# Optimization experiments

Measured on AMD Instinct MI355X. Metric: run time of the kernel, lower is better.

## Reference

```python
import jax, jax.numpy as jnp
import numpy as np

B, C, H, W, K = 16, 512, 64, 64, 64  # K = external-attention latent dim (self.k = 64)


def setup_inputs() -> dict:
    key = jax.random.key(0)
    ks = jax.random.split(key, 5)
    x = jax.random.normal(ks[0], (B, C, H, W), dtype=jnp.float32)
    # conv1: Conv2d(c, c, 1) with bias; init normal(0, sqrt(2/(1*1*out_channels)))
    conv1_w = jax.random.normal(ks[1], (C, C), dtype=jnp.float32) * np.float32(np.sqrt(2.0 / C))
    conv1_b = jnp.zeros((C,), dtype=jnp.float32)
    # linear_0: Conv1d(c, k, 1, bias=False); init normal(0, sqrt(2/out_channels))
    lin0_w = jax.random.normal(ks[2], (K, C), dtype=jnp.float32) * np.float32(np.sqrt(2.0 / K))
    # linear_1: Conv1d(k, c, 1, bias=False)
    lin1_w = jax.random.normal(ks[3], (C, K), dtype=jnp.float32) * np.float32(np.sqrt(2.0 / C))
    # conv2: Conv2d(c, c, 1, bias=False)
    conv2_w = jax.random.normal(ks[4], (C, C), dtype=jnp.float32) * np.float32(np.sqrt(2.0 / C))
    return {"x": x, "conv1_w": conv1_w, "conv1_b": conv1_b,
            "lin0_w": lin0_w, "lin1_w": lin1_w, "conv2_w": conv2_w}


def reference(x, conv1_w, conv1_b, lin0_w, lin1_w, conv2_w):
    b, c, h, w = x.shape
    n = h * w
    idn = x
    # conv1: 1x1 conv == per-pixel GEMM
    y = jnp.einsum('oc,bchw->bohw', conv1_w, x) + conv1_b[None, :, None, None]
    y = y.reshape(b, c, n)
    # external attention: linear_0 -> softmax over tokens -> L1 renorm over latent dim
    attn = jnp.einsum('kc,bcn->bkn', lin0_w, y)          # (b, K, n)
    attn = jax.nn.softmax(attn, axis=-1)
    attn = attn / (1e-9 + attn.sum(axis=1, keepdims=True))
    y = jnp.einsum('ck,bkn->bcn', lin1_w, attn)          # (b, c, n)
    # rank: view(-1, c) row-major (as torch .view does), per-row topk threshold,
    # scale below-threshold by 0.75 and the rest by 1.25; output is detached
    # (torch.tensor(pred, requires_grad=False)) -> stop_gradient
    top_k = c // 2
    flat = y.reshape(-1, c)                               # (b*n, c) row-major chunks
    thr = jax.lax.top_k(flat, top_k)[0][:, -1:]           # k-th largest per row
    scaled = jnp.where(flat < thr, 0.75 * flat, 1.25 * flat)
    yr = jax.lax.stop_gradient(scaled).reshape(b, c, h, w)
    # conv2: 1x1 conv no bias + ReLU, residual add, final ReLU
    out = jax.nn.relu(jnp.einsum('oc,bchw->bohw', conv2_w, yr))
    return jax.nn.relu(out + idn)
```

## Files before the change

### kernel.cpp

```cpp
#include <hip/hip_runtime.h>
#include <stdint.h>

typedef unsigned short u16;
typedef unsigned int u32;
using short8 = __attribute__((ext_vector_type(8))) short;
using f32x4  = __attribute__((ext_vector_type(4))) float;

#define BDIM 16
#define CDIM 512
#define KLAT 64
#define NTOK 4096

__device__ __forceinline__ u16 f2bf(float x) {
  union { float f; u32 u; } a; a.f = x;
  u32 r = a.u + 0x7FFFu + ((a.u >> 16) & 1u);
  return (u16)(r >> 16);
}
__device__ __forceinline__ u32 pack2(float a, float b) {
  return (u32)f2bf(a) | ((u32)f2bf(b) << 16);
}
__device__ __forceinline__ u32 f2key(float x) {
  u32 u = __float_as_uint(x);
  return (u & 0x80000000u) ? ~u : (u | 0x80000000u);
}
__device__ __forceinline__ float keyscale(u32 k_, u32 thr) {
  u32 u = (k_ & 0x80000000u) ? (k_ & 0x7FFFFFFFu) : ~k_;
  float v = __uint_as_float(u);
  return (k_ < thr) ? 0.75f * v : 1.25f * v;
}
__device__ __forceinline__ void gload_lds16(const void* g, void* l) {
  __builtin_amdgcn_global_load_lds(
      (const __attribute__((address_space(1))) unsigned int*)g,
      (__attribute__((address_space(3))) unsigned int*)l, 16, 0, 0);
}

__global__ __launch_bounds__(256) void k_setup(
    const float* __restrict__ conv1_w, const float* __restrict__ conv1_b,
    const float* __restrict__ lin0_w,  const float* __restrict__ lin1_w,
    const float* __restrict__ conv2_w,
    u16* __restrict__ w0bf, float* __restrict__ b0,
    u16* __restrict__ lin1bf, u16* __restrict__ cwbf)
{
  const int bid = blockIdx.x;
  const int t = threadIdx.x;
  if (bid < 128) {
    const int kb = bid & 15, cb = bid >> 4;
    const int lane = t & 63;
    int k = kb * 4 + (t >> 6);
    k = __builtin_amdgcn_readfirstlane(k);
    const int c = cb * 64 + lane;
    float acc = 0.f;
    const float* l0 = lin0_w + (size_t)k * CDIM;
    const float* cw = conv1_w + c;
#pragma unroll 4
    for (int o = 0; o < CDIM; ++o)
      acc = fmaf(l0[o], cw[(size_t)o * CDIM], acc);
    w0bf[k * CDIM + c] = f2bf(acc);
  } else if (bid == 128) {
    if (t < KLAT) {
      float acc = 0.f;
      for (int c = 0; c < CDIM; ++c) acc = fmaf(lin0_w[t * CDIM + c], conv1_b[c], acc);
      b0[t] = acc;
    }
  } else if (bid < 193) {
    const int b2 = bid - 129;
    const float4* src = (const float4*)conv2_w;
#pragma unroll
    for (int i = 0; i < 4; ++i) {
      int idx = (b2 * 256 + t) + i * 16384;
      float4 v = src[idx];
      uint2 o;
      o.x = pack2(v.x, v.y);
      o.y = pack2(v.z, v.w);
      *(uint2*)(cwbf + (size_t)idx * 4) = o;
    }
  } else {
    const int b2 = bid - 193;
#pragma unroll
    for (int i = 0; i < 4; ++i) {
      int g = b2 * 1024 + i * 256 + t;
      float4 v0 = *(const float4*)(lin1_w + (size_t)g * 8);
      float4 v1 = *(const float4*)(lin1_w + (size_t)g * 8 + 4);
      uint4 o;
      o.x = pack2(v0.x, v0.y); o.y = pack2(v0.z, v0.w);
      o.z = pack2(v1.x, v1.y); o.w = pack2(v1.z, v1.w);
      *(uint4*)(lin1bf + (size_t)g * 8) = o;
    }
  }
}

__global__ __launch_bounds__(256) void k_logits(
    const u16* __restrict__ w0bf, const float* __restrict__ x,
    const float* __restrict__ b0, float* __restrict__ logits)
{
  __shared__ u16 As[64 * 72];
  __shared__ float xt[64 * 128];
  const int nb = blockIdx.x, b = blockIdx.y;
  const int t = threadIdx.x;
  const int wv = t >> 6, lane = t & 63;
  const int quad = lane >> 4, l15 = lane & 15;
  f32x4 acc[4][2];
#pragma unroll
  for (int mi = 0; mi < 4; ++mi)
#pragma unroll
    for (int ni = 0; ni < 2; ++ni) acc[mi][ni] = (f32x4){0.f, 0.f, 0.f, 0.f};

  for (int kc = 0; kc < 8; ++kc) {
#pragma unroll
    for (int i = 0; i < 2; ++i) {
      int ch = t + i * 256;
      int row = ch >> 3, col = (ch & 7) * 8;
      uint4 a = *(const uint4*)(w0bf + (size_t)row * CDIM + kc * 64 + col);
      *(uint4*)&As[row * 72 + col] = a;
    }
#pragma unroll
    for (int i = 0; i < 8; ++i) {
      int f4 = t + i * 256;
      int row = f4 >> 5, col4 = f4 & 31;
      float4 v = *(const float4*)(x + ((size_t)(b * CDIM + kc * 64 + row)) * NTOK
                                  + nb * 128 + col4 * 4);
      int phys4 = (col4 + row + (row >> 3)) & 31;
      *(float4*)&xt[row * 128 + phys4 * 4] = v;
    }
    __syncthreads();
#pragma unroll
    for (int kk = 0; kk < 2; ++kk) {
      short8 af[4], bf_[2];
#pragma unroll
      for (int mi = 0; mi < 4; ++mi)
        af[mi] = *(short8*)&As[(mi * 16 + l15) * 72 + kk * 32 + quad * 8];
#pragma unroll
      for (int ni = 0; ni < 2; ++ni) {
        const int n = wv * 32 + ni * 16 + l15;
        const int n4 = n >> 2, ns = n & 3;
        union { u32 u[4]; short8 s; } cvt;
#pragma unroll
        for (int jj = 0; jj < 4; ++jj) {
          int ca = kk * 32 + quad * 8 + jj * 2;
          int cb2 = ca + 1;
          float v0 = xt[ca * 128 + (((n4 + ca + (ca >> 3)) & 31) * 4) + ns];
          float v1 = xt[cb2 * 128 + (((n4 + cb2 + (cb2 >> 3)) & 31) * 4) + ns];
          cvt.u[jj] = pack2(v0, v1);
        }
        bf_[ni] = cvt.s;
      }
#pragma unroll
      for (int mi = 0; mi < 4; ++mi)
#pragma unroll
        for (int ni = 0; ni < 2; ++ni)
          acc[mi][ni] = __builtin_amdgcn_mfma_f32_16x16x32_bf16(
              af[mi], bf_[ni], acc[mi][ni], 0, 0, 0);
    }
    __syncthreads();
  }
#pragma unroll
  for (int mi = 0; mi < 4; ++mi) {
#pragma unroll
    for (int ni = 0; ni < 2; ++ni) {
#pragma unroll
      for (int r = 0; r < 4; ++r) {
        int row = mi * 16 + quad * 4 + r;
        int col = nb * 128 + wv * 32 + ni * 16 + l15;
        logits[((size_t)(b * KLAT + row)) * NTOK + col] = acc[mi][ni][r] + b0[row];
      }
    }
  }
}

__global__ __launch_bounds__(256) void k_softmax(float* __restrict__ attn)
{
  __shared__ float red[4], red2[4];
  const int t = threadIdx.x;
  float* p = attn + (size_t)blockIdx.x * NTOK;
  float4 v[4];
#pragma unroll
  for (int i = 0; i < 4; ++i) v[i] = ((float4*)p)[t + i * 256];
  float m = v[0].x;
#pragma unroll
  for (int i = 0; i < 4; ++i)
    m = fmaxf(m, fmaxf(fmaxf(v[i].x, v[i].y), fmaxf(v[i].z, v[i].w)));
#pragma unroll
  for (int o = 1; o < 64; o <<= 1) m = fmaxf(m, __shfl_xor(m, o));
  const int wv = t >> 6, lane = t & 63;
  if (lane == 0) red[wv] = m;
  __syncthreads();
  m = fmaxf(fmaxf(red[0], red[1]), fmaxf(red[2], red[3]));
  float s = 0.f;
#pragma unroll
  for (int i = 0; i < 4; ++i) {
    v[i].x = __expf(v[i].x - m); s += v[i].x;
    v[i].y = __expf(v[i].y - m); s += v[i].y;
    v[i].z = __expf(v[i].z - m); s += v[i].z;
    v[i].w = __expf(v[i].w - m); s += v[i].w;
  }
#pragma unroll
  for (int o = 1; o < 64; o <<= 1) s += __shfl_xor(s, o);
  if (lane == 0) red2[wv] = s;
  __syncthreads();
  s = red2[0] + red2[1] + red2[2] + red2[3];
  const float inv = 1.f / s;
#pragma unroll
  for (int i = 0; i < 4; ++i) {
    v[i].x *= inv; v[i].y *= inv; v[i].z *= inv; v[i].w *= inv;
    ((float4*)p)[t + i * 256] = v[i];
  }
}

__global__ __launch_bounds__(256) void k_attnT(
    const float* __restrict__ attn, u16* __restrict__ attnT)
{
  __shared__ float tile[64 * 256];
  __shared__ float inv_[256];
  const int n0 = blockIdx.x * 256, b = blockIdx.y;
  const int t = threadIdx.x;
#pragma unroll
  for (int i = 0; i < 16; ++i) {
    int f4 = t + i * 256;
    int row = f4 >> 6, col4 = f4 & 63;
    float4 v = *(const float4*)(attn + ((size_t)(b * KLAT + row)) * NTOK + n0 + col4 * 4);
    int phys4 = (col4 + row + (row >> 3)) & 63;
    *(float4*)&tile[row * 256 + phys4 * 4] = v;
  }
  __syncthreads();
  {
    int n4 = t >> 2, sub = t & 3;
    float s = 0.f;
#pragma unroll
    for (int k = 0; k < 64; ++k) {
      int phys4 = (n4 + k + (k >> 3)) & 63;
      s += tile[k * 256 + phys4 * 4 + sub];
    }
    inv_[t] = 1.f / (1e-9f + s);
  }
  __syncthreads();
#pragma unroll
  for (int i = 0; i < 8; ++i) {
    int nr = (t >> 3) + i * 32;
    int cs = (t & 7) * 8;
    float sc = inv_[nr];
    float w[8];
#pragma unroll
    for (int j = 0; j < 8; ++j) {
      int row = cs + j;
      int phys4 = ((nr >> 2) + row + (row >> 3)) & 63;
      w[j] = tile[row * 256 + phys4 * 4 + (nr & 3)] * sc;
    }
    uint4 o;
    o.x = pack2(w[0], w[1]); o.y = pack2(w[2], w[3]);
    o.z = pack2(w[4], w[5]); o.w = pack2(w[6], w[7]);
    *(uint4*)(attnT + ((size_t)(b * NTOK + n0 + nr)) * KLAT + cs) = o;
  }
}

__global__ __launch_bounds__(512) void k_lin1rank(
    const u16* __restrict__ lin1bf, const u16* __restrict__ attnT,
    u16* __restrict__ yrt)
{
  __shared__ float tile[32 * 512];
  const int n0 = blockIdx.x * 512, c0 = blockIdx.y * 32, b = blockIdx.z;
  const int t = threadIdx.x;
  const int wv = t >> 6, lane = t & 63;
  const int quad = lane >> 4, l15 = lane & 15;

  short8 af[2][2], bfr[4][2];
#pragma unroll
  for (int mi = 0; mi < 2; ++mi)
#pragma unroll
    for (int kk = 0; kk < 2; ++kk)
      af[mi][kk] = *(const short8*)(lin1bf +
          (size_t)(c0 + mi * 16 + l15) * KLAT + kk * 32 + quad * 8);
#pragma unroll
  for (int ni = 0; ni < 4; ++ni)
#pragma unroll
    for (int kk = 0; kk < 2; ++kk)
      bfr[ni][kk] = *(const short8*)(attnT +
          ((size_t)(b * NTOK + n0 + wv * 64 + ni * 16 + l15)) * KLAT + kk * 32 + quad * 8);
  f32x4 acc[2][4];
#pragma unroll
  for (int mi = 0; mi < 2; ++mi)
#pragma unroll
    for (int ni = 0; ni < 4; ++ni) acc[mi][ni] = (f32x4){0.f, 0.f, 0.f, 0.f};
#pragma unroll
  for (int kk = 0; kk < 2; ++kk)
#pragma unroll
    for (int mi = 0; mi < 2; ++mi)
#pragma unroll
      for (int ni = 0; ni < 4; ++ni)
        acc[mi][ni] = __builtin_amdgcn_mfma_f32_16x16x32_bf16(
            af[mi][kk], bfr[ni][kk], acc[mi][ni], 0, 0, 0);
#pragma unroll
  for (int mi = 0; mi < 2; ++mi) {
#pragma unroll
    for (int ni = 0; ni < 4; ++ni) {
#pragma unroll
      for (int r = 0; r < 4; ++r) {
        int row = mi * 16 + quad * 4 + r;
        int col = wv * 64 + ni * 16 + l15;
        int phys4 = ((col >> 2) + row + (row >> 3)) & 127;
        tile[row * 512 + phys4 * 4 + (col & 3)] = acc[mi][ni][r];
      }
    }
  }
  __syncthreads();

#pragma unroll
  for (int r = 0; r < 4; ++r) {
    const int row = wv * 4 + r;
    const int rot = row + (row >> 3);
    const int c4a = (lane + rot) & 127;
    const int c4b = (64 + lane + rot) & 127;
    float* pa = &tile[row * 512 + c4a * 4];
    float* pb = &tile[row * 512 + c4b * 4];
    float4 va = *(const float4*)pa;
    float4 vb = *(const float4*)pb;
    u32 key[8];
    key[0] = f2key(va.x); key[1] = f2key(va.y);
    key[2] = f2key(va.z); key[3] = f2key(va.w);
    key[4] = f2key(vb.x); key[5] = f2key(vb.y);
    key[6] = f2key(vb.z); key[7] = f2key(vb.w);
    u32 kmin = key[0], kmax = key[0];
#pragma unroll
    for (int j = 1; j < 8; ++j) {
      kmin = key[j] < kmin ? key[j] : kmin;
      kmax = key[j] > kmax ? key[j] : kmax;
    }
#pragma unroll
    for (int o = 1; o < 64; o <<= 1) {
      u32 a_ = __shfl_xor(kmin, o), b_ = __shfl_xor(kmax, o);
      kmin = a_ < kmin ? a_ : kmin;
      kmax = b_ > kmax ? b_ : kmax;
    }
    u32 lo = kmin, hi = kmax;
    u32 thr;
    if (lo >= hi) thr = lo;
    else for (;;) {
      u32 d = hi - lo;
      u32 mid = lo + (d >> 1) + (d & 1u);
      int cnt = 0;
#pragma unroll
      for (int j = 0; j < 8; ++j)
        cnt += (int)__popcll(__ballot(key[j] >= mid));
      if (cnt == 256) { thr = mid; break; }
      if (cnt > 256) lo = mid; else hi = mid - 1u;
      if (lo >= hi) { thr = lo; break; }
    }
    float4 oa, ob;
    oa.x = keyscale(key[0], thr); oa.y = keyscale(key[1], thr);
    oa.z = keyscale(key[2], thr); oa.w = keyscale(key[3], thr);
    ob.x = keyscale(key[4], thr); ob.y = keyscale(key[5], thr);
    ob.z = keyscale(key[6], thr); ob.w = keyscale(key[7], thr);
    *(float4*)pa = oa;
    *(float4*)pb = ob;
  }
  __syncthreads();

#pragma unroll
  for (int i = 0; i < 4; ++i) {
    int nr = (t >> 2) + i * 128;
    int cs = (t & 3) * 8;
    float w[8];
#pragma unroll
    for (int j = 0; j < 8; ++j) {
      int row = cs + j;
      int phys4 = ((nr >> 2) + row + (row >> 3)) & 127;
      w[j] = tile[row * 512 + phys4 * 4 + (nr & 3)];
    }
    uint4 o;
    o.x = pack2(w[0], w[1]); o.y = pack2(w[2], w[3]);
    o.z = pack2(w[4], w[5]); o.w = pack2(w[6], w[7]);
    *(uint4*)(yrt + ((size_t)(b * NTOK + n0 + nr)) * CDIM + c0 + cs) = o;
  }
}

__global__ __launch_bounds__(256) void k_conv2(
    const u16* __restrict__ cwbf, const u16* __restrict__ yrt,
    const float* __restrict__ x, float* __restrict__ out)
{
  __shared__ __align__(16) u16 smem[2 * 128 * 64];
  u16* As = smem;
  u16* Bs = smem + 128 * 64;
  float* sbuf = (float*)smem;
  const int nb = blockIdx.x, mb = blockIdx.y, b = blockIdx.z;
  const int t = threadIdx.x;
  const int wv = t >> 6, lane = t & 63;
  const int wm = wv >> 1, wn = wv & 1;
  const int quad = lane >> 4, l15 = lane & 15;
  const int lrow = lane >> 3, lg = lane & 7;
  f32x4 acc[4][4];
#pragma unroll
  for (int mi = 0; mi < 4; ++mi)
#pragma unroll
    for (int ni = 0; ni < 4; ++ni) acc[mi][ni] = (f32x4){0.f, 0.f, 0.f, 0.f};

  for (int kc = 0; kc < 8; ++kc) {
#pragma unroll
    for (int i = 0; i < 4; ++i) {
      const int r0 = i * 32 + wv * 8;
      const int row = r0 + lrow;
      const int gsrc = lg ^ (row & 7);
      const u16* ga = cwbf + ((size_t)(mb * 128 + row)) * CDIM + kc * 64 + gsrc * 8;
      gload_lds16(ga, &As[r0 * 64]);
      const u16* gb = yrt + ((size_t)(b * NTOK + nb * 128 + row)) * CDIM + kc * 64 + gsrc * 8;
      gload_lds16(gb, &Bs[r0 * 64]);
    }
    __syncthreads();
#pragma unroll
    for (int kk = 0; kk < 2; ++kk) {
      short8 af[4], bf_[4];
#pragma unroll
      for (int mi = 0; mi < 4; ++mi) {
        int row = wm * 64 + mi * 16 + l15;
        int q = kk * 4 + quad;
        af[mi] = *(short8*)&As[row * 64 + ((q ^ (row & 7)) * 8)];
      }
#pragma unroll
      for (int ni = 0; ni < 4; ++ni) {
        int row = wn * 64 + ni * 16 + l15;
        int q = kk * 4 + quad;
        bf_[ni] = *(short8*)&Bs[row * 64 + ((q ^ (row & 7)) * 8)];
      }
#pragma unroll
      for (int mi = 0; mi < 4; ++mi)
#pragma unroll
        for (int ni = 0; ni < 4; ++ni)
          acc[mi][ni] = __builtin_amdgcn_mfma_f32_16x16x32_bf16(
              af[mi], bf_[ni], acc[mi][ni], 0, 0, 0);
    }
    __syncthreads();
  }
#pragma unroll
  for (int mi = 0; mi < 4; ++mi) {
#pragma unroll
    for (int ni = 0; ni < 4; ++ni)
#pragma unroll
      for (int r = 0; r < 4; ++r)
        sbuf[(wm * 16 + quad * 4 + r) * 132 + wn * 64 + ni * 16 + l15] = acc[mi][ni][r];
    __syncthreads();
#pragma unroll
    for (int i = 0; i < 4; ++i) {
      int f4 = t + i * 256;
      int sr = f4 >> 5, sc4 = f4 & 31;
      int grow = mb * 128 + (sr >> 4) * 64 + mi * 16 + (sr & 15);
      size_t off = ((size_t)(b * CDIM + grow)) * NTOK + nb * 128 + sc4 * 4;
      float4 a4 = *(const float4*)&sbuf[sr * 132 + sc4 * 4];
      float4 xa = *(const float4*)(x + off);
      float4 o4;
      o4.x = fmaxf(fmaxf(a4.x, 0.f) + xa.x, 0.f);
      o4.y = fmaxf(fmaxf(a4.y, 0.f) + xa.y, 0.f);
      o4.z = fmaxf(fmaxf(a4.z, 0.f) + xa.z, 0.f);
      o4.w = fmaxf(fmaxf(a4.w, 0.f) + xa.w, 0.f);
      *(float4*)(out + off) = o4;
    }
    __syncthreads();
  }
}

extern "C" void kernel_launch(void* const* d_in, const int* in_sizes, int n_in,
                              void* d_out, int out_size, void* d_ws, size_t ws_size,
                              hipStream_t stream)
{
  const float* x       = (const float*)d_in[0];
  const float* conv1_w = (const float*)d_in[1];
  const float* conv1_b = (const float*)d_in[2];
  const float* lin0_w  = (const float*)d_in[3];
  const float* lin1_w  = (const float*)d_in[4];
  const float* conv2_w = (const float*)d_in[5];
  float* out = (float*)d_out;

  char* ws = (char*)d_ws;
  float* attn  = (float*)ws;
  u16*   yrt   = (u16*)(ws + 16777216);
  u16*   attnT = (u16*)d_out;
  char*  wsm   = ws + 16777216 + 67108864;
  u16*   w0bf  = (u16*)wsm;
  float* b0    = (float*)(wsm + 131072);
  u16*   lin1bf= (u16*)(wsm + 131328);
  u16*   cwbf  = (u16*)(wsm + 262400);

  k_setup   <<<197, 256, 0, stream>>>(conv1_w, conv1_b, lin0_w, lin1_w, conv2_w,
                                      w0bf, b0, lin1bf, cwbf);
  k_logits  <<<dim3(32, 16), 256, 0, stream>>>(w0bf, x, b0, attn);
  k_softmax <<<1024, 256, 0, stream>>>(attn);
  k_attnT   <<<dim3(16, 16), 256, 0, stream>>>(attn, attnT);
  k_lin1rank<<<dim3(8, 16, 16), 512, 0, stream>>>(lin1bf, attnT, yrt);
  k_conv2   <<<dim3(32, 4, 16), 256, 0, stream>>>(cwbf, yrt, x, out);
}
```

Baseline: 474.0 us.

## Load conv2 MFMA operands directly from global memory, bypassing LDS staging

```diff
diff --git a/kernel.cpp b/kernel.cpp
--- a/kernel.cpp
+++ b/kernel.cpp
@@ -27,11 +27,6 @@
   u32 u = (k_ & 0x80000000u) ? (k_ & 0x7FFFFFFFu) : ~k_;
   float v = __uint_as_float(u);
   return (k_ < thr) ? 0.75f * v : 1.25f * v;
-}
-__device__ __forceinline__ void gload_lds16(const void* g, void* l) {
-  __builtin_amdgcn_global_load_lds(
-      (const __attribute__((address_space(1))) unsigned int*)g,
-      (__attribute__((address_space(3))) unsigned int*)l, 16, 0, 0);
 }
 
 __global__ __launch_bounds__(256) void k_setup(
@@ -376,58 +371,50 @@
     const u16* __restrict__ cwbf, const u16* __restrict__ yrt,
     const float* __restrict__ x, float* __restrict__ out)
 {
-  __shared__ __align__(16) u16 smem[2 * 128 * 64];
-  u16* As = smem;
-  u16* Bs = smem + 128 * 64;
-  float* sbuf = (float*)smem;
+  __shared__ __align__(16) float sbuf[32 * 132];
   const int nb = blockIdx.x, mb = blockIdx.y, b = blockIdx.z;
   const int t = threadIdx.x;
   const int wv = t >> 6, lane = t & 63;
   const int wm = wv >> 1, wn = wv & 1;
   const int quad = lane >> 4, l15 = lane & 15;
-  const int lrow = lane >> 3, lg = lane & 7;
   f32x4 acc[4][4];
 #pragma unroll
   for (int mi = 0; mi < 4; ++mi)
 #pragma unroll
     for (int ni = 0; ni < 4; ++ni) acc[mi][ni] = (f32x4){0.f, 0.f, 0.f, 0.f};
 
+  const u16* arow[4];
+  const u16* brow[4];
+#pragma unroll
+  for (int mi = 0; mi < 4; ++mi)
+    arow[mi] = cwbf + ((size_t)(mb * 128 + wm * 64 + mi * 16 + l15)) * CDIM + quad * 8;
+#pragma unroll
+  for (int ni = 0; ni < 4; ++ni)
+    brow[ni] = yrt + ((size_t)(b * NTOK + nb * 128 + wn * 64 + ni * 16 + l15)) * CDIM + quad * 8;
+
+#pragma unroll 2
   for (int kc = 0; kc < 8; ++kc) {
-#pragma unroll
-    for (int i = 0; i < 4; ++i) {
-      const int r0 = i * 32 + wv * 8;
-      const int row = r0 + lrow;
-      const int gsrc = lg ^ (row & 7);
-      const u16* ga = cwbf + ((size_t)(mb * 128 + row)) * CDIM + kc * 64 + gsrc * 8;
-      gload_lds16(ga, &As[r0 * 64]);
-      const u16* gb = yrt + ((size_t)(b * NTOK + nb * 128 + row)) * CDIM + kc * 64 + gsrc * 8;
-      gload_lds16(gb, &Bs[r0 * 64]);
-    }
-    __syncthreads();
-#pragma unroll
-    for (int kk = 0; kk < 2; ++kk) {
-      short8 af[4], bf_[4];
-#pragma unroll
-      for (int mi = 0; mi < 4; ++mi) {
-        int row = wm * 64 + mi * 16 + l15;
-        int q = kk * 4 + quad;
-        af[mi] = *(short8*)&As[row * 64 + ((q ^ (row & 7)) * 8)];
-      }
-#pragma unroll
-      for (int ni = 0; ni < 4; ++ni) {
-        int row = wn * 64 + ni * 16 + l15;
-        int q = kk * 4 + quad;
-        bf_[ni] = *(short8*)&Bs[row * 64 + ((q ^ (row & 7)) * 8)];
-      }
+    short8 af[4][2], bf_[4][2];
+#pragma unroll
+    for (int mi = 0; mi < 4; ++mi) {
+      af[mi][0] = *(const short8*)(arow[mi] + kc * 64);
+      af[mi][1] = *(const short8*)(arow[mi] + kc * 64 + 32);
+    }
+#pragma unroll
+    for (int ni = 0; ni < 4; ++ni) {
+      bf_[ni][0] = *(const short8*)(brow[ni] + kc * 64);
+      bf_[ni][1] = *(const short8*)(brow[ni] + kc * 64 + 32);
+    }
+#pragma unroll
+    for (int kk = 0; kk < 2; ++kk)
 #pragma unroll
       for (int mi = 0; mi < 4; ++mi)
 #pragma unroll
         for (int ni = 0; ni < 4; ++ni)
           acc[mi][ni] = __builtin_amdgcn_mfma_f32_16x16x32_bf16(
-              af[mi], bf_[ni], acc[mi][ni], 0, 0, 0);
-    }
-    __syncthreads();
-  }
+              af[mi][kk], bf_[ni][kk], acc[mi][ni], 0, 0, 0);
+  }
+
 #pragma unroll
   for (int mi = 0; mi < 4; ++mi) {
 #pragma unroll
```

Measured after the change: 553.9 us. 16.9% more time.
